# Performance work log

Measured on AMD Instinct MI355X. Metric: run time of the kernel, lower is better.

Reference implementation:

```python
import jax, jax.numpy as jnp
import numpy as np

B, F_CH, K, N = 8, 512, 8, 2048

def sl3_basis():
    # Chevalley-style basis of sl(3,R): 2 diagonal (traceless) + 6 off-diagonal generators
    E = np.zeros((8, 3, 3), np.float32)
    E[0] = [[1, 0, 0], [0, -1, 0], [0, 0, 0]]
    E[1] = [[0, 1, 0], [0, 0, 0], [0, 0, 0]]
    E[2] = [[0, 0, 1], [0, 0, 0], [0, 0, 0]]
    E[3] = [[0, 0, 0], [1, 0, 0], [0, 0, 0]]
    E[4] = [[0, 0, 0], [0, 1, 0], [0, 0, -1]]
    E[5] = [[0, 0, 0], [0, 0, 1], [0, 0, 0]]
    E[6] = [[0, 0, 0], [0, 0, 0], [1, 0, 0]]
    E[7] = [[0, 0, 0], [0, 0, 0], [0, 1, 0]]
    return jnp.asarray(E)

def setup_inputs() -> dict:
    key = jax.random.key(0)
    kx, kw = jax.random.split(key)
    x = jax.random.normal(kx, (B, F_CH, K, N), dtype=jnp.float32)
    # learn_dir = nn.Linear(F, F, bias=False); weight is [out, in]
    W = jax.random.normal(kw, (F_CH, F_CH), dtype=jnp.float32) * (1.0 / np.sqrt(F_CH))
    return {"x": x, "W": W}

def reference(x, W):
    # x: [B, F, 8, N]; W: [F, F]
    E = sl3_basis()                                   # [8, 3, 3]
    # Killing form of sl(3): K(X, Y) = 6 * tr(X Y). Since hat() is linear in v,
    # K(hat(a), hat(b)) = a^T G b with Gram matrix G_ab = 6 * tr(E_a E_b).
    G = 6.0 * jnp.einsum('aij,bji->ab', E, E)         # [8, 8]
    # learn_dir applied over channel axis F (equivalent to transpose(1,-1) + Linear)
    d = jnp.einsum('bfkn,gf->bgkn', x, W)             # [B, F, 8, N]
    # killing form of x_hat with d_hat, per (b, f, n)
    kf = jnp.einsum('bfkn,kl,bfln->bfn', x, G, d)[:, :, None, :]  # [B, F, 1, N]
    # torch.where(kf <= 0, x, x - -kf * d)  ==  x + kf * d on the positive branch
    return jnp.where(kf <= 0, x, x + kf * d)
```

## Files before the change

### kernel.cpp

```cpp
#include <hip/hip_runtime.h>


typedef short bf16x8 __attribute__((ext_vector_type(8)));
typedef short bf16x4 __attribute__((ext_vector_type(4)));
typedef float f32x4 __attribute__((ext_vector_type(4)));

__device__ __forceinline__ unsigned short f2bf(float f) {
  unsigned int u = __float_as_uint(f);
  u += 0x7fffu + ((u >> 16) & 1u);
  return (unsigned short)(u >> 16);
}

__device__ __forceinline__ float bfu(unsigned short u) {
  return __uint_as_float(((unsigned int)u) << 16);
}

__global__ __launch_bounds__(256) void prepack_w(const float* __restrict__ W,
                                                 short* __restrict__ wp) {
  const int cid = blockIdx.x * 256 + threadIdx.x;
  const int row  = cid & 511;
  const int kgkt = cid >> 9;
  const int kg = kgkt & 3;
  const int kt = kgkt >> 2;
  const float* src = W + (size_t)row * 512 + kt * 32 + kg * 8;
  bf16x8 v;
#pragma unroll
  for (int j = 0; j < 8; ++j) v[j] = (short)f2bf(src[j]);
  *(bf16x8*)&wp[(size_t)cid * 8] = v;
}

__global__ __launch_bounds__(1024, 4) void lnkill_fullg6(
    const float* __restrict__ x, const short* __restrict__ wp,
    float* __restrict__ out) {
  __shared__ __align__(16) short ldsX[16][4096];

  const int tid   = threadIdx.x;
  const int lane  = tid & 63;
  const int w     = tid >> 6;
  const int klane = lane >> 4;
  const int li    = lane & 15;

  const int bid = blockIdx.x;
  const int nt  = bid & 127;
  const int b   = bid >> 7;
  const int n0  = nt * 16;

  const int kgs = tid >> 8;
  const int cm  = (tid >> 1) & 127;
  const int j0  = (tid & 1) * 4;
  const float* xs = x + (((size_t)(b * 512 + kgs * 8 + j0)) * 8 + (cm >> 4)) * 2048
                      + n0 + (cm & 15);
  const int bwr = tid * 4;

  f32x4 acc[2][8] = {};
  float rB[2][4];

#pragma unroll
  for (int jj = 0; jj < 4; ++jj) rB[0][jj] = xs[(size_t)jj * 16384];
#pragma unroll
  for (int jj = 0; jj < 4; ++jj) rB[1][jj] = xs[(size_t)(32 + jj) * 16384];
#pragma unroll
  for (int t = 0; t < 8; ++t) {
    bf16x4 v;
#pragma unroll
    for (int jj = 0; jj < 4; ++jj) v[jj] = (short)f2bf(rB[t & 1][jj]);
    *(bf16x4*)&ldsX[t][bwr] = v;
#pragma unroll
    for (int jj = 0; jj < 4; ++jj)
      rB[t & 1][jj] = xs[(size_t)((t + 2) * 32 + jj) * 16384];
  }
  __syncthreads();

#pragma unroll
  for (int kt = 0; kt < 8; ++kt) {
    {
      bf16x4 v;
#pragma unroll
      for (int jj = 0; jj < 4; ++jj) v[jj] = (short)f2bf(rB[kt & 1][jj]);
      *(bf16x4*)&ldsX[kt + 8][bwr] = v;
    }
    if (kt < 6) {
#pragma unroll
      for (int jj = 0; jj < 4; ++jj)
        rB[kt & 1][jj] = xs[(size_t)((kt + 10) * 32 + jj) * 16384];
    }
    const short* wt = wp + ((size_t)(kt * 4 + klane) * 512 + w * 32 + li) * 8;
    bf16x8 afr0 = *(const bf16x8*)(wt);
    bf16x8 afr1 = *(const bf16x8*)(wt + 128);
    const short* Bc = ldsX[kt];
#pragma unroll
    for (int fn = 0; fn < 8; ++fn) {
      bf16x8 bfr = *(const bf16x8*)&Bc[(klane * 128 + fn * 16 + li) * 8];
      acc[0][fn] = __builtin_amdgcn_mfma_f32_16x16x32_bf16(afr0, bfr,
                                                           acc[0][fn], 0, 0, 0);
      acc[1][fn] = __builtin_amdgcn_mfma_f32_16x16x32_bf16(afr1, bfr,
                                                           acc[1][fn], 0, 0, 0);
    }
  }
  __syncthreads();

#pragma unroll
  for (int kt = 8; kt < 16; ++kt) {
    const short* wt = wp + ((size_t)(kt * 4 + klane) * 512 + w * 32 + li) * 8;
    bf16x8 afr0 = *(const bf16x8*)(wt);
    bf16x8 afr1 = *(const bf16x8*)(wt + 128);
    const short* Bc = ldsX[kt];
#pragma unroll
    for (int fn = 0; fn < 8; ++fn) {
      bf16x8 bfr = *(const bf16x8*)&Bc[(klane * 128 + fn * 16 + li) * 8];
      acc[0][fn] = __builtin_amdgcn_mfma_f32_16x16x32_bf16(afr0, bfr,
                                                           acc[0][fn], 0, 0, 0);
      acc[1][fn] = __builtin_amdgcn_mfma_f32_16x16x32_bf16(afr1, bfr,
                                                           acc[1][fn], 0, 0, 0);
    }
  }

  const unsigned short* xls = (const unsigned short*)&ldsX[w][0];
#pragma unroll
  for (int fm = 0; fm < 2; ++fm) {
#pragma unroll
    for (int r = 0; r < 4; ++r) {
      const int g = w * 32 + fm * 16 + klane * 4 + r;
      const size_t base = ((size_t)(b * 512 + g)) * 16384 + n0 + li;
      const int kgd = fm * 2 + (klane >> 1);
      const int jd  = (klane & 1) * 4 + r;
      float xk[8];
#pragma unroll
      for (int k = 0; k < 8; ++k)
        xk[k] = bfu(xls[(kgd * 128 + k * 16 + li) * 8 + jd]);
      const float c0 = 12.f * xk[0] - 6.f * xk[4];
      const float c4 = 12.f * xk[4] - 6.f * xk[0];
      const float c1 = 6.f * xk[3];
      const float c2 = 6.f * xk[6];
      const float c3 = 6.f * xk[1];
      const float c5 = 6.f * xk[7];
      const float c6 = 6.f * xk[2];
      const float c7 = 6.f * xk[5];
      const float kf = c0 * acc[fm][0][r] + c1 * acc[fm][1][r]
                     + c2 * acc[fm][2][r] + c3 * acc[fm][3][r]
                     + c4 * acc[fm][4][r] + c5 * acc[fm][5][r]
                     + c6 * acc[fm][6][r] + c7 * acc[fm][7][r];
#pragma unroll
      for (int k = 0; k < 8; ++k) {
        const float o = (kf <= 0.f) ? xk[k] : fmaf(kf, acc[fm][k][r], xk[k]);
        out[base + (size_t)k * 2048] = o;
      }
    }
  }
}

__global__ __launch_bounds__(512, 4) void lnkill_fused(
    const float* __restrict__ x, const float* __restrict__ W,
    float* __restrict__ out) {
  __shared__ __align__(16) short ldsA[2][4096];
  __shared__ __align__(16) short ldsB[2][4096];

  const int tid  = threadIdx.x;
  const int lane = tid & 63;
  const int w    = tid >> 6;

  const int bid = blockIdx.x;
  const int l   = (bid & 7) * 512 + (bid >> 3);
  const int gt  = l & 3;
  const int nt  = (l >> 2) & 127;
  const int b   = l >> 9;
  const int g0  = gt * 128;
  const int n0  = nt * 16;

  const int cm = tid & 127;
  const int fg = tid >> 7;
  const float* xs   = x + (((size_t)(b * 512 + fg * 8)) * 8 + (cm >> 4)) * 2048
                        + n0 + (cm & 15);
  const float* Wrow = W + (size_t)(g0 + cm) * 512 + fg * 8;

  f32x4 acc[8] = {};

  {
    float xv[8];
#pragma unroll
    for (int j = 0; j < 8; ++j) xv[j] = xs[(size_t)j * 16384];
    float4 wv[2];
    const float4* wpp = (const float4*)Wrow;
    wv[0] = wpp[0]; wv[1] = wpp[1];
    const float* wf = (const float*)wv;
    bf16x8 vb, va;
#pragma unroll
    for (int j = 0; j < 8; ++j) {
      vb[j] = (short)f2bf(xv[j]);
      va[j] = (short)f2bf(wf[j]);
    }
    *(bf16x8*)&ldsB[0][(fg * 128 + cm) * 8] = vb;
    *(bf16x8*)&ldsA[0][(fg * 128 + cm) * 8] = va;
  }
  __syncthreads();

  const int klane = lane >> 4;
  const int li    = lane & 15;

  for (int kt = 0; kt < 16; ++kt) {
    const int cur = kt & 1;
    float xv[8];
    float4 wv[2];
    if (kt < 15) {
      const float* xpn = xs + (size_t)(kt + 1) * 32 * 16384;
#pragma unroll
      for (int j = 0; j < 8; ++j) xv[j] = xpn[(size_t)j * 16384];
      const float4* wpp = (const float4*)(Wrow + (kt + 1) * 32);
      wv[0] = wpp[0]; wv[1] = wpp[1];
    }
    {
      const short* Ac = ldsA[cur];
      const short* Bc = ldsB[cur];
      bf16x8 afr = *(const bf16x8*)&Ac[(klane * 128 + w * 16 + li) * 8];
#pragma unroll
      for (int fn = 0; fn < 8; ++fn) {
        bf16x8 bfr = *(const bf16x8*)&Bc[(klane * 128 + fn * 16 + li) * 8];
        acc[fn] = __builtin_amdgcn_mfma_f32_16x16x32_bf16(afr, bfr, acc[fn], 0, 0, 0);
      }
    }
    if (kt < 15) {
      const int nxt = cur ^ 1;
      const float* wf = (const float*)wv;
      bf16x8 vb, va;
#pragma unroll
      for (int j = 0; j < 8; ++j) {
        vb[j] = (short)f2bf(xv[j]);
        va[j] = (short)f2bf(wf[j]);
      }
      __syncthreads();
      *(bf16x8*)&ldsB[nxt][(fg * 128 + cm) * 8] = vb;
      *(bf16x8*)&ldsA[nxt][(fg * 128 + cm) * 8] = va;
      __syncthreads();
    }
  }

#pragma unroll
  for (int r = 0; r < 4; ++r) {
    const int g = g0 + w * 16 + klane * 4 + r;
    const size_t base = ((size_t)(b * 512 + g)) * 16384 + n0 + li;
    float xk[8];
#pragma unroll
    for (int k = 0; k < 8; ++k) xk[k] = x[base + (size_t)k * 2048];
    const float c0 = 12.f * xk[0] - 6.f * xk[4];
    const float c4 = 12.f * xk[4] - 6.f * xk[0];
    const float c1 = 6.f * xk[3];
    const float c2 = 6.f * xk[6];
    const float c3 = 6.f * xk[1];
    const float c5 = 6.f * xk[7];
    const float c6 = 6.f * xk[2];
    const float c7 = 6.f * xk[5];
    const float kf = c0 * acc[0][r] + c1 * acc[1][r]
                   + c2 * acc[2][r] + c3 * acc[3][r]
                   + c4 * acc[4][r] + c5 * acc[5][r]
                   + c6 * acc[6][r] + c7 * acc[7][r];
#pragma unroll
    for (int k = 0; k < 8; ++k) {
      const float o = (kf <= 0.f) ? xk[k] : fmaf(kf, acc[k][r], xk[k]);
      out[base + (size_t)k * 2048] = o;
    }
  }
}

extern "C" void kernel_launch(void* const* d_in, const int* in_sizes, int n_in,
                              void* d_out, int out_size, void* d_ws, size_t ws_size,
                              hipStream_t stream) {
  const float* x = (const float*)d_in[0];
  const float* W = (const float*)d_in[1];
  float* out = (float*)d_out;

  if (ws_size >= (size_t)524288) {
    short* wp = (short*)d_ws;
    prepack_w<<<dim3(128), dim3(256), 0, stream>>>(W, wp);
    lnkill_fullg6<<<dim3(1024), dim3(1024), 0, stream>>>(x, wp, out);
  } else {
    lnkill_fused<<<dim3(4096), dim3(512), 0, stream>>>(x, W, out);
  }
}
```

Baseline: 175.2 us.

## Split output channels across two 512-thread blocks with streamed half-K buffering

Each workgroup now computes half of the output channels (256) for a 16-column tile instead of all 512, using 512 threads and 2048 blocks. It keeps its own half of the input channels resident in LDS for the epilogue and streams the other half through a two-slot double buffer, cutting LDS from 128KB to 80KB so more blocks can be resident. A bijective block-index swizzle is added. The cost is that each x tile is read from global memory twice (once per half) and there are more barriers per K step.

```diff
diff --git a/kernel.cpp b/kernel.cpp
--- a/kernel.cpp
+++ b/kernel.cpp
@@ -2,7 +2,6 @@
 
 
 typedef short bf16x8 __attribute__((ext_vector_type(8)));
-typedef short bf16x4 __attribute__((ext_vector_type(4)));
 typedef float f32x4 __attribute__((ext_vector_type(4)));
 
 __device__ __forceinline__ unsigned short f2bf(float f) {
@@ -29,10 +28,10 @@
   *(bf16x8*)&wp[(size_t)cid * 8] = v;
 }
 
-__global__ __launch_bounds__(1024, 4) void lnkill_fullg6(
+__global__ __launch_bounds__(512, 4) void lnkill_halfg(
     const float* __restrict__ x, const short* __restrict__ wp,
     float* __restrict__ out) {
-  __shared__ __align__(16) short ldsX[16][4096];
+  __shared__ __align__(16) short lds[10][4096];
 
   const int tid   = threadIdx.x;
   const int lane  = tid & 63;
@@ -41,86 +40,101 @@
   const int li    = lane & 15;
 
   const int bid = blockIdx.x;
-  const int nt  = bid & 127;
-  const int b   = bid >> 7;
+  const int l   = (bid & 7) * 256 + (bid >> 3);
+  const int h   = l & 1;
+  const int nt  = (l >> 1) & 127;
+  const int b   = l >> 8;
   const int n0  = nt * 16;
-
-  const int kgs = tid >> 8;
-  const int cm  = (tid >> 1) & 127;
-  const int j0  = (tid & 1) * 4;
-  const float* xs = x + (((size_t)(b * 512 + kgs * 8 + j0)) * 8 + (cm >> 4)) * 2048
+  const int g0  = h * 256;
+
+  const int ownk = 8 * h;
+  const int othk = 8 * (1 - h);
+
+  const int kgs = tid >> 7;
+  const int cm  = tid & 127;
+  const float* xs = x + (((size_t)(b * 512 + kgs * 8)) * 8 + (cm >> 4)) * 2048
                       + n0 + (cm & 15);
-  const int bwr = tid * 4;
+  const int bwr = tid * 8;
 
   f32x4 acc[2][8] = {};
-  float rB[2][4];
-
-#pragma unroll
-  for (int jj = 0; jj < 4; ++jj) rB[0][jj] = xs[(size_t)jj * 16384];
-#pragma unroll
-  for (int jj = 0; jj < 4; ++jj) rB[1][jj] = xs[(size_t)(32 + jj) * 16384];
+  float rB[8];
+
 #pragma unroll
   for (int t = 0; t < 8; ++t) {
-    bf16x4 v;
-#pragma unroll
-    for (int jj = 0; jj < 4; ++jj) v[jj] = (short)f2bf(rB[t & 1][jj]);
-    *(bf16x4*)&ldsX[t][bwr] = v;
-#pragma unroll
-    for (int jj = 0; jj < 4; ++jj)
-      rB[t & 1][jj] = xs[(size_t)((t + 2) * 32 + jj) * 16384];
-  }
+#pragma unroll
+    for (int j = 0; j < 8; ++j)
+      rB[j] = xs[(size_t)((ownk + t) * 32 + j) * 16384];
+    bf16x8 v;
+#pragma unroll
+    for (int j = 0; j < 8; ++j) v[j] = (short)f2bf(rB[j]);
+    *(bf16x8*)&lds[t][bwr] = v;
+  }
+  {
+#pragma unroll
+    for (int j = 0; j < 8; ++j)
+      rB[j] = xs[(size_t)(othk * 32 + j) * 16384];
+    bf16x8 v;
+#pragma unroll
+    for (int j = 0; j < 8; ++j) v[j] = (short)f2bf(rB[j]);
+    *(bf16x8*)&lds[8][bwr] = v;
+  }
+#pragma unroll
+  for (int j = 0; j < 8; ++j)
+    rB[j] = xs[(size_t)((othk + 1) * 32 + j) * 16384];
   __syncthreads();
 
 #pragma unroll
-  for (int kt = 0; kt < 8; ++kt) {
+  for (int o = 0; o < 8; ++o) {
+    if (o < 7) {
+      bf16x8 v;
+#pragma unroll
+      for (int j = 0; j < 8; ++j) v[j] = (short)f2bf(rB[j]);
+      *(bf16x8*)&lds[8 + ((o + 1) & 1)][bwr] = v;
+      if (o < 6) {
+#pragma unroll
+        for (int j = 0; j < 8; ++j)
+          rB[j] = xs[(size_t)((othk + o + 2) * 32 + j) * 16384];
+      }
+    }
     {
-      bf16x4 v;
-#pragma unroll
-      for (int jj = 0; jj < 4; ++jj) v[jj] = (short)f2bf(rB[kt & 1][jj]);
-      *(bf16x4*)&ldsX[kt + 8][bwr] = v;
-    }
-    if (kt < 6) {
-#pragma unroll
-      for (int jj = 0; jj < 4; ++jj)
-        rB[kt & 1][jj] = xs[(size_t)((kt + 10) * 32 + jj) * 16384];
-    }
-    const short* wt = wp + ((size_t)(kt * 4 + klane) * 512 + w * 32 + li) * 8;
-    bf16x8 afr0 = *(const bf16x8*)(wt);
-    bf16x8 afr1 = *(const bf16x8*)(wt + 128);
-    const short* Bc = ldsX[kt];
-#pragma unroll
-    for (int fn = 0; fn < 8; ++fn) {
-      bf16x8 bfr = *(const bf16x8*)&Bc[(klane * 128 + fn * 16 + li) * 8];
-      acc[0][fn] = __builtin_amdgcn_mfma_f32_16x16x32_bf16(afr0, bfr,
-                                                           acc[0][fn], 0, 0, 0);
-      acc[1][fn] = __builtin_amdgcn_mfma_f32_16x16x32_bf16(afr1, bfr,
-                                                           acc[1][fn], 0, 0, 0);
-    }
-  }
-  __syncthreads();
-
-#pragma unroll
-  for (int kt = 8; kt < 16; ++kt) {
-    const short* wt = wp + ((size_t)(kt * 4 + klane) * 512 + w * 32 + li) * 8;
-    bf16x8 afr0 = *(const bf16x8*)(wt);
-    bf16x8 afr1 = *(const bf16x8*)(wt + 128);
-    const short* Bc = ldsX[kt];
-#pragma unroll
-    for (int fn = 0; fn < 8; ++fn) {
-      bf16x8 bfr = *(const bf16x8*)&Bc[(klane * 128 + fn * 16 + li) * 8];
-      acc[0][fn] = __builtin_amdgcn_mfma_f32_16x16x32_bf16(afr0, bfr,
-                                                           acc[0][fn], 0, 0, 0);
-      acc[1][fn] = __builtin_amdgcn_mfma_f32_16x16x32_bf16(afr1, bfr,
-                                                           acc[1][fn], 0, 0, 0);
-    }
-  }
-
-  const unsigned short* xls = (const unsigned short*)&ldsX[w][0];
+      const short* wt = wp + ((size_t)((ownk + o) * 4 + klane) * 512
+                              + g0 + w * 32 + li) * 8;
+      bf16x8 afr0 = *(const bf16x8*)(wt);
+      bf16x8 afr1 = *(const bf16x8*)(wt + 128);
+      const short* Bc = lds[o];
+#pragma unroll
+      for (int fn = 0; fn < 8; ++fn) {
+        bf16x8 bfr = *(const bf16x8*)&Bc[(klane * 128 + fn * 16 + li) * 8];
+        acc[0][fn] = __builtin_amdgcn_mfma_f32_16x16x32_bf16(afr0, bfr,
+                                                             acc[0][fn], 0, 0, 0);
+        acc[1][fn] = __builtin_amdgcn_mfma_f32_16x16x32_bf16(afr1, bfr,
+                                                             acc[1][fn], 0, 0, 0);
+      }
+    }
+    {
+      const short* wt = wp + ((size_t)((othk + o) * 4 + klane) * 512
+                              + g0 + w * 32 + li) * 8;
+      bf16x8 afr0 = *(const bf16x8*)(wt);
+      bf16x8 afr1 = *(const bf16x8*)(wt + 128);
+      const short* Bc = lds[8 + (o & 1)];
+#pragma unroll
+      for (int fn = 0; fn < 8; ++fn) {
+        bf16x8 bfr = *(const bf16x8*)&Bc[(klane * 128 + fn * 16 + li) * 8];
+        acc[0][fn] = __builtin_amdgcn_mfma_f32_16x16x32_bf16(afr0, bfr,
+                                                             acc[0][fn], 0, 0, 0);
+        acc[1][fn] = __builtin_amdgcn_mfma_f32_16x16x32_bf16(afr1, bfr,
+                                                             acc[1][fn], 0, 0, 0);
+      }
+    }
+    if (o < 7) __syncthreads();
+  }
+
+  const unsigned short* xls = (const unsigned short*)&lds[w][0];
 #pragma unroll
   for (int fm = 0; fm < 2; ++fm) {
 #pragma unroll
     for (int r = 0; r < 4; ++r) {
-      const int g = w * 32 + fm * 16 + klane * 4 + r;
+      const int g = g0 + w * 32 + fm * 16 + klane * 4 + r;
       const size_t base = ((size_t)(b * 512 + g)) * 16384 + n0 + li;
       const int kgd = fm * 2 + (klane >> 1);
       const int jd  = (klane & 1) * 4 + r;
@@ -142,8 +156,8 @@
                      + c6 * acc[fm][6][r] + c7 * acc[fm][7][r];
 #pragma unroll
       for (int k = 0; k < 8; ++k) {
-        const float o = (kf <= 0.f) ? xk[k] : fmaf(kf, acc[fm][k][r], xk[k]);
-        out[base + (size_t)k * 2048] = o;
+        const float o2 = (kf <= 0.f) ? xk[k] : fmaf(kf, acc[fm][k][r], xk[k]);
+        out[base + (size_t)k * 2048] = o2;
       }
     }
   }
@@ -271,7 +285,7 @@
   if (ws_size >= (size_t)524288) {
     short* wp = (short*)d_ws;
     prepack_w<<<dim3(128), dim3(256), 0, stream>>>(W, wp);
-    lnkill_fullg6<<<dim3(1024), dim3(1024), 0, stream>>>(x, wp, out);
+    lnkill_halfg<<<dim3(2048), dim3(512), 0, stream>>>(x, wp, out);
   } else {
     lnkill_fused<<<dim3(4096), dim3(512), 0, stream>>>(x, W, out);
   }
```

New measurement: 237.6 us. 35.6% more time.
